# Kernel tuning notes

Measured on AMD Instinct MI355X. Metric: run time of the kernel, lower is better.

## Reference

```python
import jax, jax.numpy as jnp
from jax import lax
import numpy as np

IC, S, TS = 16, 3, 2  # inter_channels, num_subset_S, num_subset_T
EPS = 1e-5

def _ln2(x, g, b):
    # LayerNorm over last two dims (torch normalized_shape=[D1, D2])
    m = x.mean((-2, -1), keepdims=True)
    v = ((x - m) ** 2).mean((-2, -1), keepdims=True)
    return (x - m) / jnp.sqrt(v + EPS) * g + b

def _gelu(x):
    return jax.nn.gelu(x, approximate=False)

def setup_inputs() -> dict:
    key = jax.random.key(0)
    ks = jax.random.split(key, 12)
    N, V, T, C = 128, 25, 64, 64
    f = jnp.float32
    d = {}
    d['x'] = jax.random.normal(ks[0], (N, V, T, C), f)
    # spatial attention
    d['w_in_s'] = jax.random.normal(ks[1], (C, 2 * S * IC), f) * 0.05
    d['b_in_s'] = jnp.zeros((2 * S * IC,), f)
    d['alphas'] = jnp.ones((1, 1, 1, S), f)
    d['attention0s'] = jnp.ones((1, V, V, S), f) / V
    d['w_out_s'] = jax.random.normal(ks[2], (S * C, C), f) * 0.05
    d['b_out_s'] = jnp.zeros((C,), f)
    d['ln_out_s_g'] = jnp.ones((T, C), f)
    d['ln_out_s_b'] = jnp.zeros((T, C), f)
    d['w_ff_s'] = jax.random.normal(ks[3], (C, C), f) * 0.05
    d['b_ff_s'] = jnp.zeros((C,), f)
    d['ln_ff_s_g'] = jnp.ones((T, C), f)
    d['ln_ff_s_b'] = jnp.zeros((T, C), f)
    # temporal (directed) attention
    d['w_in_t'] = jax.random.normal(ks[4], (C, 4 * TS * IC), f) * 0.05
    d['b_in_t'] = jnp.zeros((4 * TS * IC,), f)
    d['alphat_f'] = jnp.ones((1, 1, 1, TS), f)
    d['alphat_b'] = jnp.ones((1, 1, 1, TS), f)
    d['w_out_t'] = jax.random.normal(ks[5], (2 * TS * C, C), f) * 0.05
    d['b_out_t'] = jnp.zeros((C,), f)
    d['ln_out_t_g'] = jnp.ones((V, C), f)
    d['ln_out_t_b'] = jnp.zeros((V, C), f)
    d['w_ff_t'] = jax.random.normal(ks[6], (C, C), f) * 0.05
    d['b_ff_t'] = jnp.zeros((C,), f)
    d['ln_ff_t_g'] = jnp.ones((V, C), f)
    d['ln_ff_t_b'] = jnp.zeros((V, C), f)
    # TCN tail: Conv2d(C, C, (7,1), pad (3,0)) + BatchNorm2d
    d['conv_w'] = jax.random.normal(ks[7], (C, C, 7, 1), f) * 0.05
    d['conv_b'] = jnp.zeros((C,), f)
    d['bn_g'] = jnp.ones((C,), f)
    d['bn_b'] = jnp.zeros((C,), f)
    return d

def reference(x, w_in_s, b_in_s, alphas, attention0s, w_out_s, b_out_s,
              ln_out_s_g, ln_out_s_b, w_ff_s, b_ff_s, ln_ff_s_g, ln_ff_s_b,
              w_in_t, b_in_t, alphat_f, alphat_b, w_out_t, b_out_t,
              ln_out_t_g, ln_out_t_b, w_ff_t, b_ff_t, ln_ff_t_g, ln_ff_t_b,
              conv_w, conv_b, bn_g, bn_b):
    N, V, T, C = x.shape
    # ---- spatial attention (tanh scores + global bias) ----
    qk = (x @ w_in_s + b_in_s).reshape(N, V, T, IC, 2 * S)
    q, k = qk[..., :S], qk[..., S:]
    att = jnp.tanh(jnp.einsum('nutcs,nvtcs->nuvs', q, k) / (IC * T)) * alphas + attention0s
    y = jnp.einsum('nutc,nuvs->nvtcs', x, att).reshape(N, V, T, S * C)
    y = _ln2(y @ w_out_s + b_out_s, ln_out_s_g, ln_out_s_b)
    y = _gelu(x + y)
    y = _gelu(x + _ln2(y @ w_ff_s + b_ff_s, ln_ff_s_g, ln_ff_s_b))
    y = y.transpose(0, 2, 1, 3)  # (N, T, V, C)
    # ---- directed temporal attention (causal masks) ----
    qkt = (y @ w_in_t + b_in_t).reshape(N, T, V, IC, 4 * TS)
    q_f, q_b = qkt[..., 0:TS], qkt[..., TS:2 * TS]
    k_f, k_b = qkt[..., 2 * TS:3 * TS], qkt[..., 3 * TS:]
    bmask = jnp.triu(jnp.ones((T, T), x.dtype))  # backward mask
    fmask = bmask.T                               # forward mask
    att_b = jnp.tanh(jnp.einsum('ntvcs,nqvcs->ntqs', q_b, k_b) / (IC * V)) * alphat_b
    att_f = jnp.tanh(jnp.einsum('ntvcs,nqvcs->ntqs', q_f, k_f) / (IC * V)) * alphat_f
    att_b = att_b * bmask[None, :, :, None]
    att_f = att_f * fmask[None, :, :, None]
    z_f = jnp.einsum('ntvc,ntqs->nqvcs', y, att_f).reshape(N, T, V, TS * C)
    z_b = jnp.einsum('ntvc,ntqs->nqvcs', y, att_b).reshape(N, T, V, TS * C)
    z = jnp.concatenate([z_f, z_b], axis=-1)  # (N, T, V, 2*TS*C)
    z = _ln2(z @ w_out_t + b_out_t, ln_out_t_g, ln_out_t_b)
    z = _gelu(y + z)
    z = _gelu(y + _ln2(z @ w_ff_t + b_ff_t, ln_ff_t_g, ln_ff_t_b))
    # ---- TCN tail: (N,T,V,C) -> (N,C,T,V) conv over T ----
    zc = z.transpose(0, 3, 1, 2)
    z1 = lax.conv_general_dilated(zc, conv_w, (1, 1), [(3, 3), (0, 0)],
                                  dimension_numbers=('NCHW', 'OIHW', 'NCHW'))
    z1 = z1 + conv_b[None, :, None, None]
    m = z1.mean((0, 2, 3), keepdims=True)
    v = ((z1 - m) ** 2).mean((0, 2, 3), keepdims=True)
    z1 = (z1 - m) / jnp.sqrt(v + EPS) * bn_g[None, :, None, None] + bn_b[None, :, None, None]
    z = _gelu(zc + z1)
    return z.transpose(0, 3, 2, 1)  # (N, C, T, V) -> (N, V, T, C)
```

## Files before the change

kernel.cpp:

```cpp
#include <hip/hip_runtime.h>
#include <math.h>

namespace {

constexpr int V_ = 25, T_ = 64, C_ = 64;

__device__ __forceinline__ float gelu_f(float x) {
  return 0.5f * x * (1.0f + erff(x * 0.7071067811865475f));
}

__device__ __forceinline__ float block_sum(float v, float* red, int tid) {
  red[tid] = v; __syncthreads();
#pragma unroll
  for (int o = 128; o > 0; o >>= 1) {
    if (tid < o) red[tid] += red[tid + o];
    __syncthreads();
  }
  float r = red[0]; __syncthreads();
  return r;
}

template <int NC>
__launch_bounds__(256, 2)
__global__ void gemm_k64(const float* __restrict__ A, const float* __restrict__ B,
                         const float* __restrict__ bias, float* __restrict__ C) {
  __shared__ float Al[64 * 68];
  __shared__ float Bl[64 * (NC + 4)];
  const int tid = threadIdx.x;
  const int row0 = blockIdx.x * 64;
  for (int i = tid; i < 4096; i += 256)
    Al[(i >> 6) * 68 + (i & 63)] = A[(size_t)(row0 + (i >> 6)) * 64 + (i & 63)];
  for (int i = tid; i < 64 * NC; i += 256) {
    int k = i / NC, c = i - k * NC;
    Bl[k * (NC + 4) + c] = B[i];
  }
  __syncthreads();
  const int ri = tid >> 5, cg = tid & 31;
  if (cg * 4 < NC) {
    float4 acc[8];
    float4 bf = *(const float4*)&bias[cg * 4];
#pragma unroll
    for (int i = 0; i < 8; ++i) acc[i] = bf;
    for (int k0 = 0; k0 < 64; k0 += 4) {
      float4 bv0 = *(const float4*)&Bl[(k0 + 0) * (NC + 4) + cg * 4];
      float4 bv1 = *(const float4*)&Bl[(k0 + 1) * (NC + 4) + cg * 4];
      float4 bv2 = *(const float4*)&Bl[(k0 + 2) * (NC + 4) + cg * 4];
      float4 bv3 = *(const float4*)&Bl[(k0 + 3) * (NC + 4) + cg * 4];
#pragma unroll
      for (int i = 0; i < 8; ++i) {
        float4 av = *(const float4*)&Al[(ri * 8 + i) * 68 + k0];
        acc[i].x += av.x * bv0.x + av.y * bv1.x + av.z * bv2.x + av.w * bv3.x;
        acc[i].y += av.x * bv0.y + av.y * bv1.y + av.z * bv2.y + av.w * bv3.y;
        acc[i].z += av.x * bv0.z + av.y * bv1.z + av.z * bv2.z + av.w * bv3.z;
        acc[i].w += av.x * bv0.w + av.y * bv1.w + av.z * bv2.w + av.w * bv3.w;
      }
    }
#pragma unroll
    for (int i = 0; i < 8; ++i)
      *(float4*)&C[(size_t)(row0 + ri * 8 + i) * NC + cg * 4] = acc[i];
  }
}

__global__ void att_s_kernel(const float* __restrict__ qk, const float* __restrict__ alphas,
                             const float* __restrict__ att0, float* __restrict__ att) {
  __shared__ float qs[4 * 3072];
  __shared__ float ks[3072];
  const int b = blockIdx.x, tid = threadIdx.x;
  const int n = b / 7, ug = b % 7;
  const int u0 = ug * 4;
  const int nu = (25 - u0 < 4) ? (25 - u0) : 4;
  for (int i = tid; i < nu * 3072; i += 256) {
    int ul = i / 3072, r = i - ul * 3072;
    int s = r >> 10, idx = r & 1023, t = idx >> 4, c = idx & 15;
    qs[i] = qk[(size_t)(n * 25 + u0 + ul) * 6144 + t * 96 + c * 6 + s];
  }
  const int ui = tid >> 6, l = tid & 63;
  const int u = u0 + ui;
  const float a0 = alphas[0], a1 = alphas[1], a2 = alphas[2];
  for (int v = 0; v < 25; ++v) {
    __syncthreads();
    for (int i = tid; i < 3072; i += 256) {
      int s = i >> 10, idx = i & 1023, t = idx >> 4, c = idx & 15;
      ks[i] = qk[(size_t)(n * 25 + v) * 6144 + t * 96 + c * 6 + 3 + s];
    }
    __syncthreads();
    if (u < 25) {
      float s0 = 0.f, s1 = 0.f, s2 = 0.f;
      for (int idx = l; idx < 1024; idx += 64) {
        s0 += qs[ui * 3072 + idx] * ks[idx];
        s1 += qs[ui * 3072 + 1024 + idx] * ks[1024 + idx];
        s2 += qs[ui * 3072 + 2048 + idx] * ks[2048 + idx];
      }
#pragma unroll
      for (int o = 32; o > 0; o >>= 1) {
        s0 += __shfl_down(s0, o);
        s1 += __shfl_down(s1, o);
        s2 += __shfl_down(s2, o);
      }
      if (l == 0) {
        float* dst = &att[(size_t)((n * 25 + u) * 25 + v) * 3];
        const float* ap = &att0[(u * 25 + v) * 3];
        dst[0] = tanhf(s0 * (1.f / 1024.f)) * a0 + ap[0];
        dst[1] = tanhf(s1 * (1.f / 1024.f)) * a1 + ap[1];
        dst[2] = tanhf(s2 * (1.f / 1024.f)) * a2 + ap[2];
      }
    }
  }
}

__launch_bounds__(256, 2)
__global__ void mix_gemm_s(const float* __restrict__ x, const float* __restrict__ att,
                           const float* __restrict__ w, const float* __restrict__ bias,
                           float* __restrict__ y2) {
  __shared__ float la[1875];
  __shared__ float xs[1600];
  __shared__ float y1l[25 * 194];
  __shared__ float wl[192 * 36];
  const int b = blockIdx.x, tid = threadIdx.x;
  const int n = b >> 6, t = b & 63;
  for (int i = tid; i < 1875; i += 256) la[i] = att[(size_t)n * 1875 + i];
  for (int i = tid; i < 1600; i += 256) {
    int u = i >> 6, c = i & 63;
    xs[i] = x[(size_t)((n * 25 + u) * 64 + t) * 64 + c];
  }
  __syncthreads();
  for (int slot = tid; slot < 400; slot += 256) {
    int v = slot >> 4, cg = slot & 15;
    float4 s0 = {0, 0, 0, 0}, s1 = {0, 0, 0, 0}, s2 = {0, 0, 0, 0};
    for (int u = 0; u < 25; ++u) {
      float4 xv = *(const float4*)&xs[u * 64 + cg * 4];
      const float* lp = &la[(u * 25 + v) * 3];
      float w0 = lp[0], w1 = lp[1], w2 = lp[2];
      s0.x += xv.x * w0; s0.y += xv.y * w0; s0.z += xv.z * w0; s0.w += xv.w * w0;
      s1.x += xv.x * w1; s1.y += xv.y * w1; s1.z += xv.z * w1; s1.w += xv.w * w1;
      s2.x += xv.x * w2; s2.y += xv.y * w2; s2.z += xv.z * w2; s2.w += xv.w * w2;
    }
    float* yp = &y1l[v * 194 + cg * 12];
    yp[0] = s0.x; yp[1] = s1.x; yp[2] = s2.x;
    yp[3] = s0.y; yp[4] = s1.y; yp[5] = s2.y;
    yp[6] = s0.z; yp[7] = s1.z; yp[8] = s2.z;
    yp[9] = s0.w; yp[10] = s1.w; yp[11] = s2.w;
  }
  for (int h = 0; h < 2; ++h) {
    __syncthreads();
    for (int i = tid; i < 192 * 32; i += 256) {
      int k = i >> 5, cc = i & 31;
      wl[k * 36 + cc] = w[k * 64 + h * 32 + cc];
    }
    __syncthreads();
    if (tid < 200) {
      int v = tid >> 3, cp = tid & 7;
      float4 acc = *(const float4*)&bias[h * 32 + cp * 4];
      for (int k = 0; k < 192; ++k) {
        float yv = y1l[v * 194 + k];
        float4 wv = *(const float4*)&wl[k * 36 + cp * 4];
        acc.x += yv * wv.x; acc.y += yv * wv.y; acc.z += yv * wv.z; acc.w += yv * wv.w;
      }
      *(float4*)&y2[(size_t)((n * 25 + v) * 64 + t) * 64 + h * 32 + cp * 4] = acc;
    }
  }
}

__global__ void lnln_s_kernel(const float* __restrict__ y2, const float* __restrict__ x,
                              const float* __restrict__ wff, const float* __restrict__ bff,
                              const float* __restrict__ g1, const float* __restrict__ b1,
                              const float* __restrict__ g2, const float* __restrict__ b2,
                              float* __restrict__ yt) {
  __shared__ float ya[64 * 66];
  __shared__ float wl[64 * 68];
  __shared__ float y6l[64 * 68];
  __shared__ float red[256];
  const int g = blockIdx.x, tid = threadIdx.x;
  const int n = g / 25, v = g % 25;
  const size_t base = (size_t)g * 4096;
  float s = 0.f;
  for (int i = tid; i < 4096; i += 256) {
    float val = y2[base + i];
    ya[(i >> 6) * 66 + (i & 63)] = val;
    s += val;
  }
  for (int i = tid; i < 4096; i += 256) wl[(i >> 6) * 68 + (i & 63)] = wff[i];
  float mean = block_sum(s, red, tid) * (1.f / 4096.f);
  float sq = 0.f;
  for (int i = tid; i < 4096; i += 256) {
    float d = ya[(i >> 6) * 66 + (i & 63)] - mean;
    sq += d * d;
  }
  float inv = rsqrtf(block_sum(sq, red, tid) * (1.f / 4096.f) + 1e-5f);
  for (int i = tid; i < 4096; i += 256) {
    int o = (i >> 6) * 66 + (i & 63);
    ya[o] = gelu_f(x[base + i] + (ya[o] - mean) * inv * g1[i] + b1[i]);
  }
  __syncthreads();
  const int ri = tid >> 4, ci = tid & 15;
  {
    float4 bf = *(const float4*)&bff[ci * 4];
    float4 acc[4];
#pragma unroll
    for (int i = 0; i < 4; ++i) acc[i] = bf;
    for (int k = 0; k < 64; ++k) {
      float4 wv = *(const float4*)&wl[k * 68 + ci * 4];
#pragma unroll
      for (int i = 0; i < 4; ++i) {
        float av = ya[(ri + 16 * i) * 66 + k];
        acc[i].x += av * wv.x; acc[i].y += av * wv.y;
        acc[i].z += av * wv.z; acc[i].w += av * wv.w;
      }
    }
#pragma unroll
    for (int i = 0; i < 4; ++i)
      *(float4*)&y6l[(ri + 16 * i) * 68 + ci * 4] = acc[i];
  }
  __syncthreads();
  float s2 = 0.f;
  for (int i = tid; i < 4096; i += 256) s2 += y6l[(i >> 6) * 68 + (i & 63)];
  float mean2 = block_sum(s2, red, tid) * (1.f / 4096.f);
  float sq2 = 0.f;
  for (int i = tid; i < 4096; i += 256) {
    float d = y6l[(i >> 6) * 68 + (i & 63)] - mean2;
    sq2 += d * d;
  }
  float inv2 = rsqrtf(block_sum(sq2, red, tid) * (1.f / 4096.f) + 1e-5f);
  for (int i = tid; i < 4096; i += 256) {
    int t = i >> 6, c = i & 63;
    yt[(size_t)((n * 64 + t) * 25 + v) * 64 + c] =
        gelu_f(x[base + i] + (y6l[t * 68 + c] - mean2) * inv2 * g2[i] + b2[i]);
  }
}

__global__ void att_t_kernel(const float* __restrict__ qkt, const float* __restrict__ af_al,
                             const float* __restrict__ ab_al, float* __restrict__ att4) {
  __shared__ float qs[8 * 1600];
  __shared__ float ks[1600];
  const int b = blockIdx.x, tid = threadIdx.x;
  const int n = b >> 3, to = b & 7;
  for (int i = tid; i < 8 * 1600; i += 256) {
    int tt = i / 1600, r = i - tt * 1600;
    int pair = r >> 2, j = r & 3, v = pair >> 4, c = pair & 15;
    qs[i] = qkt[(size_t)((n * 64 + to * 8 + tt) * 25 + v) * 128 + c * 8 + j];
  }
  const int tt = tid >> 5, l = tid & 31;
  const int t = to * 8 + tt;
  const float af0 = af_al[0], af1 = af_al[1], ab0 = ab_al[0], ab1 = ab_al[1];
  for (int q = 0; q < 64; ++q) {
    __syncthreads();
    for (int i = tid; i < 1600; i += 256) {
      int pair = i >> 2, j = i & 3, v = pair >> 4, c = pair & 15;
      ks[i] = qkt[(size_t)((n * 64 + q) * 25 + v) * 128 + c * 8 + 4 + j];
    }
    __syncthreads();
    float f0 = 0.f, f1 = 0.f, b0 = 0.f, b1 = 0.f;
    for (int idx = l; idx < 400; idx += 32) {
      float4 q4 = *(const float4*)&qs[tt * 1600 + idx * 4];
      float4 k4 = *(const float4*)&ks[idx * 4];
      f0 += q4.x * k4.x; f1 += q4.y * k4.y;
      b0 += q4.z * k4.z; b1 += q4.w * k4.w;
    }
#pragma unroll
    for (int o = 16; o > 0; o >>= 1) {
      f0 += __shfl_down(f0, o, 32); f1 += __shfl_down(f1, o, 32);
      b0 += __shfl_down(b0, o, 32); b1 += __shfl_down(b1, o, 32);
    }
    if (l == 0) {
      float mf = (q <= t) ? 1.f : 0.f;
      float mb = (q >= t) ? 1.f : 0.f;
      size_t o4 = ((size_t)(n * 4 + 0) * 64 + t) * 64 + q;
      att4[o4]           = tanhf(f0 * (1.f / 400.f)) * af0 * mf;
      att4[o4 + 4096]    = tanhf(f1 * (1.f / 400.f)) * af1 * mf;
      att4[o4 + 2 * 4096] = tanhf(b0 * (1.f / 400.f)) * ab0 * mb;
      att4[o4 + 3 * 4096] = tanhf(b1 * (1.f / 400.f)) * ab1 * mb;
    }
  }
}

__launch_bounds__(256, 2)
__global__ void mix_gemm_t(const float* __restrict__ yt, const float* __restrict__ att4,
                           const float* __restrict__ w, const float* __restrict__ bias,
                           float* __restrict__ z2) {
  __shared__ float smem[12288];
  float* as4 = smem;
  float* ys = smem + 8192;
  float* zvl = smem;
  const int b = blockIdx.x, tid = threadIdx.x;
  const int n = b / 50, r = b % 50;
  const int v = r >> 1, qh = r & 1;
  const int q0b = qh * 32;
  for (int i = tid; i < 8192; i += 256) {
    int sdi = i >> 11, t = (i >> 5) & 63, qq = i & 31;
    as4[i] = att4[((size_t)(n * 4 + sdi) * 64 + t) * 64 + q0b + qq];
  }
  for (int i = tid; i < 4096; i += 256) {
    int t = i >> 6, c = i & 63;
    ys[i] = yt[(size_t)((n * 64 + t) * 25 + v) * 64 + c];
  }
  __syncthreads();
  const int qg = tid >> 4, cg = tid & 15;
  const int q0 = qg * 2, c0 = cg * 4;
  float4 a00 = {0,0,0,0}, a01 = {0,0,0,0}, a10 = {0,0,0,0}, a11 = {0,0,0,0};
  float4 a20 = {0,0,0,0}, a21 = {0,0,0,0}, a30 = {0,0,0,0}, a31 = {0,0,0,0};
  for (int t = 0; t < 64; ++t) {
    float4 bv = *(const float4*)&ys[t * 64 + c0];
    float2 av0 = *(const float2*)&as4[(0 * 64 + t) * 32 + q0];
    float2 av1 = *(const float2*)&as4[(1 * 64 + t) * 32 + q0];
    float2 av2 = *(const float2*)&as4[(2 * 64 + t) * 32 + q0];
    float2 av3 = *(const float2*)&as4[(3 * 64 + t) * 32 + q0];
#define FMA4S(A, S) A.x += bv.x * (S); A.y += bv.y * (S); A.z += bv.z * (S); A.w += bv.w * (S)
    FMA4S(a00, av0.x); FMA4S(a01, av0.y);
    FMA4S(a10, av1.x); FMA4S(a11, av1.y);
    FMA4S(a20, av2.x); FMA4S(a21, av2.y);
    FMA4S(a30, av3.x); FMA4S(a31, av3.y);
#undef FMA4S
  }
  __syncthreads();
#define STORE_ZV(A, SDI, QI)                                                     \
  { int cb = ((SDI) >= 2 ? 128 : 0) + ((SDI) & 1);                               \
    float* zp = &zvl[(q0 + (QI)) * 258 + cb];                                    \
    zp[(c0 + 0) * 2] = A.x; zp[(c0 + 1) * 2] = A.y;                              \
    zp[(c0 + 2) * 2] = A.z; zp[(c0 + 3) * 2] = A.w; }
  STORE_ZV(a00, 0, 0); STORE_ZV(a01, 0, 1);
  STORE_ZV(a10, 1, 0); STORE_ZV(a11, 1, 1);
  STORE_ZV(a20, 2, 0); STORE_ZV(a21, 2, 1);
  STORE_ZV(a30, 3, 0); STORE_ZV(a31, 3, 1);
#undef STORE_ZV
  __syncthreads();
  const int qg2 = tid >> 6, cp = tid & 63;
  float acc2[8] = {0, 0, 0, 0, 0, 0, 0, 0};
  for (int col = 0; col < 256; ++col) {
    float wv = w[col * 64 + cp];
#pragma unroll
    for (int qi = 0; qi < 8; ++qi) acc2[qi] += zvl[(qg2 * 8 + qi) * 258 + col] * wv;
  }
  float bb = bias[cp];
#pragma unroll
  for (int qi = 0; qi < 8; ++qi)
    z2[(size_t)((n * 64 + q0b + qg2 * 8 + qi) * 25 + v) * 64 + cp] = acc2[qi] + bb;
}

__global__ void lnln_t_kernel(const float* __restrict__ z2, const float* __restrict__ ytr,
                              const float* __restrict__ wff, const float* __restrict__ bff,
                              const float* __restrict__ g1, const float* __restrict__ b1,
                              const float* __restrict__ g2, const float* __restrict__ b2,
                              float* __restrict__ zf) {
  __shared__ float za[25 * 66];
  __shared__ float yts[25 * 66];
  __shared__ float wl[64 * 68];
  __shared__ float z6l[25 * 68];
  __shared__ float red[256];
  const int g = blockIdx.x, tid = threadIdx.x;
  const size_t base = (size_t)g * 1600;
  float s = 0.f;
  for (int i = tid; i < 1600; i += 256) {
    float val = z2[base + i];
    za[(i >> 6) * 66 + (i & 63)] = val;
    yts[(i >> 6) * 66 + (i & 63)] = ytr[base + i];
    s += val;
  }
  for (int i = tid; i < 4096; i += 256) wl[(i >> 6) * 68 + (i & 63)] = wff[i];
  float mean = block_sum(s, red, tid) * (1.f / 1600.f);
  float sq = 0.f;
  for (int i = tid; i < 1600; i += 256) {
    float d = za[(i >> 6) * 66 + (i & 63)] - mean;
    sq += d * d;
  }
  float inv = rsqrtf(block_sum(sq, red, tid) * (1.f / 1600.f) + 1e-5f);
  for (int i = tid; i < 1600; i += 256) {
    int o = (i >> 6) * 66 + (i & 63);
    za[o] = gelu_f(yts[o] + (za[o] - mean) * inv * g1[i] + b1[i]);
  }
  __syncthreads();
  for (int slot = tid; slot < 400; slot += 256) {
    int v = slot >> 4, cq = slot & 15;
    float4 acc = *(const float4*)&bff[cq * 4];
    for (int k = 0; k < 64; ++k) {
      float av = za[v * 66 + k];
      float4 wv = *(const float4*)&wl[k * 68 + cq * 4];
      acc.x += av * wv.x; acc.y += av * wv.y; acc.z += av * wv.z; acc.w += av * wv.w;
    }
    *(float4*)&z6l[v * 68 + cq * 4] = acc;
  }
  __syncthreads();
  float s2 = 0.f;
  for (int i = tid; i < 1600; i += 256) s2 += z6l[(i >> 6) * 68 + (i & 63)];
  float mean2 = block_sum(s2, red, tid) * (1.f / 1600.f);
  float sq2 = 0.f;
  for (int i = tid; i < 1600; i += 256) {
    float d = z6l[(i >> 6) * 68 + (i & 63)] - mean2;
    sq2 += d * d;
  }
  float inv2 = rsqrtf(block_sum(sq2, red, tid) * (1.f / 1600.f) + 1e-5f);
  for (int i = tid; i < 1600; i += 256) {
    int o = (i >> 6) * 68 + (i & 63);
    zf[base + i] = gelu_f(yts[(i >> 6) * 66 + (i & 63)] + (z6l[o] - mean2) * inv2 * g2[i] + b2[i]);
  }
}

__global__ void convw_transpose(const float* __restrict__ w, float* __restrict__ wT) {
  int idx = blockIdx.x * 256 + threadIdx.x;
  if (idx < 64 * 64 * 7) {
    int dt = idx % 7, c = (idx / 7) % 64, cp = idx / 448;
    wT[(dt * 64 + c) * 64 + cp] = w[idx];
  }
}

__launch_bounds__(256, 2)
__global__ void conv_gemm(const float* __restrict__ zf, const float* __restrict__ wT,
                          const float* __restrict__ cb, float* __restrict__ z1,
                          float* __restrict__ part) {
  __shared__ float Al[128 * 68];
  __shared__ float Bl[64 * 68];
  const int tid = threadIdx.x;
  const int r0 = blockIdx.x * 128;
  const int ri = tid >> 4;
  const int cg = tid & 15;
  float4 acc[8];
  float4 bf = *(const float4*)&cb[cg * 4];
#pragma unroll
  for (int i = 0; i < 8; ++i) acc[i] = bf;
  for (int dt = 0; dt < 7; ++dt) {
    __syncthreads();
    for (int i = tid; i < 8192; i += 256) {
      int rl = i >> 6, c = i & 63;
      int grow = r0 + rl;
      int t = (grow % 1600) / 25;
      int tt = t + dt - 3;
      float val = 0.f;
      if (tt >= 0 && tt < 64)
        val = zf[(size_t)(grow + (dt - 3) * 25) * 64 + c];
      Al[rl * 68 + c] = val;
    }
    for (int i = tid; i < 4096; i += 256)
      Bl[(i >> 6) * 68 + (i & 63)] = wT[dt * 4096 + i];
    __syncthreads();
    for (int k0 = 0; k0 < 64; k0 += 4) {
      float4 bv0 = *(const float4*)&Bl[(k0 + 0) * 68 + cg * 4];
      float4 bv1 = *(const float4*)&Bl[(k0 + 1) * 68 + cg * 4];
      float4 bv2 = *(const float4*)&Bl[(k0 + 2) * 68 + cg * 4];
      float4 bv3 = *(const float4*)&Bl[(k0 + 3) * 68 + cg * 4];
#pragma unroll
      for (int i = 0; i < 8; ++i) {
        float4 av = *(const float4*)&Al[(ri + 16 * i) * 68 + k0];
        acc[i].x += av.x * bv0.x + av.y * bv1.x + av.z * bv2.x + av.w * bv3.x;
        acc[i].y += av.x * bv0.y + av.y * bv1.y + av.z * bv2.y + av.w * bv3.y;
        acc[i].z += av.x * bv0.z + av.y * bv1.z + av.z * bv2.z + av.w * bv3.z;
        acc[i].w += av.x * bv0.w + av.y * bv1.w + av.z * bv2.w + av.w * bv3.w;
      }
    }
  }
  float4 psum = {0, 0, 0, 0}, psq = {0, 0, 0, 0};
#pragma unroll
  for (int i = 0; i < 8; ++i) {
    *(float4*)&z1[(size_t)(r0 + ri + 16 * i) * 64 + cg * 4] = acc[i];
    psum.x += acc[i].x; psum.y += acc[i].y; psum.z += acc[i].z; psum.w += acc[i].w;
    psq.x += acc[i].x * acc[i].x; psq.y += acc[i].y * acc[i].y;
    psq.z += acc[i].z * acc[i].z; psq.w += acc[i].w * acc[i].w;
  }
  __syncthreads();
  *(float4*)&Al[ri * 68 + cg * 4] = psum;
  *(float4*)&Bl[ri * 68 + cg * 4] = psq;
  __syncthreads();
  if (tid < 64) {
    float s = 0.f, q = 0.f;
    for (int r = 0; r < 16; ++r) {
      s += Al[r * 68 + tid];
      q += Bl[r * 68 + tid];
    }
    part[(size_t)blockIdx.x * 128 + tid] = s;
    part[(size_t)blockIdx.x * 128 + 64 + tid] = q;
  }
}

__global__ void bn_final(const float* __restrict__ part, const float* __restrict__ g,
                         const float* __restrict__ bb, float* __restrict__ sc) {
  __shared__ float red[256], red2[256];
  const int c = blockIdx.x;
  const int tid = threadIdx.x;
  float s = 0.f, q = 0.f;
  for (int i = tid; i < 1600; i += 256) {
    s += part[(size_t)i * 128 + c];
    q += part[(size_t)i * 128 + 64 + c];
  }
  red[tid] = s;
  red2[tid] = q;
  __syncthreads();
#pragma unroll
  for (int o = 128; o > 0; o >>= 1) {
    if (tid < o) { red[tid] += red[tid + o]; red2[tid] += red2[tid + o]; }
    __syncthreads();
  }
  if (tid == 0) {
    const float M = 204800.f;
    float mean = red[0] / M;
    float var = red2[0] / M - mean * mean;
    float scale = g[c] * rsqrtf(var + 1e-5f);
    sc[c] = scale;
    sc[64 + c] = bb[c] - mean * scale;
  }
}

__global__ void final_kernel(const float* __restrict__ zf, const float* __restrict__ z1,
                             const float* __restrict__ sc, float* __restrict__ out) {
  const int b = blockIdx.x;
  const int n = b / 64, t = b % 64;
  const int tid = threadIdx.x;
  const size_t base = (size_t)(n * 64 + t) * 1600;
  for (int i = tid; i < 1600; i += 256) {
    int v = i >> 6, c = i & 63;
    float val = zf[base + i] + z1[base + i] * sc[c] + sc[64 + c];
    out[(size_t)((n * 25 + v) * 64 + t) * 64 + c] = gelu_f(val);
  }
}

}

extern "C" void kernel_launch(void* const* d_in, const int* in_sizes, int n_in,
                              void* d_out, int out_size, void* d_ws, size_t ws_size,
                              hipStream_t stream) {
  (void)in_sizes; (void)n_in; (void)out_size; (void)ws_size;
  const float* x          = (const float*)d_in[0];
  const float* w_in_s     = (const float*)d_in[1];
  const float* b_in_s     = (const float*)d_in[2];
  const float* alphas     = (const float*)d_in[3];
  const float* att0s      = (const float*)d_in[4];
  const float* w_out_s    = (const float*)d_in[5];
  const float* b_out_s    = (const float*)d_in[6];
  const float* ln_out_s_g = (const float*)d_in[7];
  const float* ln_out_s_b = (const float*)d_in[8];
  const float* w_ff_s     = (const float*)d_in[9];
  const float* b_ff_s     = (const float*)d_in[10];
  const float* ln_ff_s_g  = (const float*)d_in[11];
  const float* ln_ff_s_b  = (const float*)d_in[12];
  const float* w_in_t     = (const float*)d_in[13];
  const float* b_in_t     = (const float*)d_in[14];
  const float* alphat_f   = (const float*)d_in[15];
  const float* alphat_b   = (const float*)d_in[16];
  const float* w_out_t    = (const float*)d_in[17];
  const float* b_out_t    = (const float*)d_in[18];
  const float* ln_out_t_g = (const float*)d_in[19];
  const float* ln_out_t_b = (const float*)d_in[20];
  const float* w_ff_t     = (const float*)d_in[21];
  const float* b_ff_t     = (const float*)d_in[22];
  const float* ln_ff_t_g  = (const float*)d_in[23];
  const float* ln_ff_t_b  = (const float*)d_in[24];
  const float* conv_w     = (const float*)d_in[25];
  const float* conv_b     = (const float*)d_in[26];
  const float* bn_g       = (const float*)d_in[27];
  const float* bn_b       = (const float*)d_in[28];
  float* out = (float*)d_out;
  float* ws = (float*)d_ws;

  float* att4 = ws;
  float* part = ws;
  float* wT   = ws + 1048576;
  float* bnsc = ws + 1080000;
  float* qk   = ws + 2097152;
  float* y2   = ws + 2097152;
  float* qkt  = ws + 2097152;
  float* z1b  = ws + 2097152;
  float* yt   = ws + 28311552;
  float* zf   = ws + 41418752;
  float* att_s = out;
  float* z2    = out;

  dim3 blk(256);
  gemm_k64<96><<<3200, blk, 0, stream>>>(x, w_in_s, b_in_s, qk);
  att_s_kernel<<<128 * 7, blk, 0, stream>>>(qk, alphas, att0s, att_s);
  mix_gemm_s<<<8192, blk, 0, stream>>>(x, att_s, w_out_s, b_out_s, y2);
  lnln_s_kernel<<<3200, blk, 0, stream>>>(y2, x, w_ff_s, b_ff_s, ln_out_s_g, ln_out_s_b,
                                          ln_ff_s_g, ln_ff_s_b, yt);
  gemm_k64<128><<<3200, blk, 0, stream>>>(yt, w_in_t, b_in_t, qkt);
  att_t_kernel<<<128 * 8, blk, 0, stream>>>(qkt, alphat_f, alphat_b, att4);
  mix_gemm_t<<<6400, blk, 0, stream>>>(yt, att4, w_out_t, b_out_t, z2);
  lnln_t_kernel<<<8192, blk, 0, stream>>>(z2, yt, w_ff_t, b_ff_t, ln_out_t_g, ln_out_t_b,
                                          ln_ff_t_g, ln_ff_t_b, zf);
  convw_transpose<<<112, blk, 0, stream>>>(conv_w, wT);
  conv_gemm<<<1600, blk, 0, stream>>>(zf, wT, conv_b, z1b, part);
  bn_final<<<64, blk, 0, stream>>>(part, bn_g, bn_b, bnsc);
  final_kernel<<<8192, blk, 0, stream>>>(zf, z1b, bnsc, out);
}
```

Baseline: 2.596 ms.

## Split attention-mix and output projection into separate mix and tiled GEMM kernels

```diff
diff --git a/kernel.cpp b/kernel.cpp
--- a/kernel.cpp
+++ b/kernel.cpp
@@ -2,8 +2,6 @@
 #include <math.h>
 
 namespace {
-
-constexpr int V_ = 25, T_ = 64, C_ = 64;
 
 __device__ __forceinline__ float gelu_f(float x) {
   return 0.5f * x * (1.0f + erff(x * 0.7071067811865475f));
@@ -61,6 +59,76 @@
   }
 }
 
+template <int KT>
+__launch_bounds__(256, 3)
+__global__ void gemm_kn(const float* __restrict__ A, const float* __restrict__ Bp,
+                        const float* __restrict__ bias, float* __restrict__ C) {
+  __shared__ float Al[128 * 68];
+  __shared__ float Bl[64 * 68];
+  const int tid = threadIdx.x;
+  const int r0 = blockIdx.x * 128;
+  const int rowg = tid >> 3, colg = tid & 7, c0 = colg * 8;
+  float4 acc[4][2];
+  {
+    float4 b0 = *(const float4*)&bias[c0];
+    float4 b1 = *(const float4*)&bias[c0 + 4];
+#pragma unroll
+    for (int i = 0; i < 4; ++i) { acc[i][0] = b0; acc[i][1] = b1; }
+  }
+  for (int kc = 0; kc < KT / 64; ++kc) {
+    __syncthreads();
+    for (int i = tid; i < 8192; i += 256) {
+      int rl = i >> 6, k = i & 63;
+      Al[rl * 68 + k] = A[(size_t)(r0 + rl) * KT + kc * 64 + k];
+    }
+    for (int i = tid; i < 4096; i += 256)
+      Bl[(i >> 6) * 68 + (i & 63)] = Bp[(size_t)kc * 4096 + i];
+    __syncthreads();
+    for (int k0 = 0; k0 < 64; k0 += 4) {
+      float4 bb[4][2];
+#pragma unroll
+      for (int k = 0; k < 4; ++k) {
+        bb[k][0] = *(const float4*)&Bl[(k0 + k) * 68 + c0];
+        bb[k][1] = *(const float4*)&Bl[(k0 + k) * 68 + c0 + 4];
+      }
+#pragma unroll
+      for (int i = 0; i < 4; ++i) {
+        float4 av = *(const float4*)&Al[(rowg + 32 * i) * 68 + k0];
+#pragma unroll
+        for (int h = 0; h < 2; ++h) {
+          acc[i][h].x += av.x * bb[0][h].x + av.y * bb[1][h].x + av.z * bb[2][h].x + av.w * bb[3][h].x;
+          acc[i][h].y += av.x * bb[0][h].y + av.y * bb[1][h].y + av.z * bb[2][h].y + av.w * bb[3][h].y;
+          acc[i][h].z += av.x * bb[0][h].z + av.y * bb[1][h].z + av.z * bb[2][h].z + av.w * bb[3][h].z;
+          acc[i][h].w += av.x * bb[0][h].w + av.y * bb[1][h].w + av.z * bb[2][h].w + av.w * bb[3][h].w;
+        }
+      }
+    }
+  }
+#pragma unroll
+  for (int i = 0; i < 4; ++i) {
+    *(float4*)&C[(size_t)(r0 + rowg + 32 * i) * 64 + c0] = acc[i][0];
+    *(float4*)&C[(size_t)(r0 + rowg + 32 * i) * 64 + c0 + 4] = acc[i][1];
+  }
+}
+
+__global__ void permute_ws_k(const float* __restrict__ w, float* __restrict__ wp) {
+  int i = blockIdx.x * 256 + threadIdx.x;
+  if (i < 12288) {
+    int row = i >> 6, cc = i & 63;
+    int s = row >> 6, c = row & 63;
+    wp[i] = w[(c * 3 + s) * 64 + cc];
+  }
+}
+
+__global__ void permute_wt_k(const float* __restrict__ w, float* __restrict__ wp) {
+  int i = blockIdx.x * 256 + threadIdx.x;
+  if (i < 16384) {
+    int row = i >> 6, cc = i & 63;
+    int dir = row >> 7, r2 = row & 127, s = r2 >> 6, c = r2 & 63;
+    wp[i] = w[(dir * 128 + c * 2 + s) * 64 + cc];
+  }
+}
+
 __global__ void att_s_kernel(const float* __restrict__ qk, const float* __restrict__ alphas,
                              const float* __restrict__ att0, float* __restrict__ att) {
   __shared__ float qs[4 * 3072];
@@ -108,55 +176,58 @@
   }
 }
 
-__launch_bounds__(256, 2)
-__global__ void mix_gemm_s(const float* __restrict__ x, const float* __restrict__ att,
-                           const float* __restrict__ w, const float* __restrict__ bias,
-                           float* __restrict__ y2) {
-  __shared__ float la[1875];
-  __shared__ float xs[1600];
-  __shared__ float y1l[25 * 194];
-  __shared__ float wl[192 * 36];
+__launch_bounds__(256, 3)
+__global__ void mix_s_y1(const float* __restrict__ x, const float* __restrict__ att,
+                         float* __restrict__ y1) {
+  __shared__ float ap[625 * 4];
+  __shared__ float xs[4 * 25 * 68];
   const int b = blockIdx.x, tid = threadIdx.x;
-  const int n = b >> 6, t = b & 63;
-  for (int i = tid; i < 1875; i += 256) la[i] = att[(size_t)n * 1875 + i];
-  for (int i = tid; i < 1600; i += 256) {
-    int u = i >> 6, c = i & 63;
-    xs[i] = x[(size_t)((n * 25 + u) * 64 + t) * 64 + c];
-  }
-  __syncthreads();
-  for (int slot = tid; slot < 400; slot += 256) {
-    int v = slot >> 4, cg = slot & 15;
-    float4 s0 = {0, 0, 0, 0}, s1 = {0, 0, 0, 0}, s2 = {0, 0, 0, 0};
+  const int n = b >> 4, tq = b & 15;
+  for (int i = tid; i < 1875; i += 256) {
+    int u = i / 75, rem = i - u * 75, v = rem / 3, s = rem - v * 3;
+    ap[(v * 25 + u) * 4 + s] = att[(size_t)n * 1875 + i];
+  }
+  for (int i = tid; i < 6400; i += 256) {
+    int tl = i / 1600, r = i - tl * 1600, u = r >> 6, c = r & 63;
+    xs[(tl * 25 + u) * 68 + c] = x[(size_t)((n * 25 + u) * 64 + tq * 4 + tl) * 64 + c];
+  }
+  __syncthreads();
+  if (tid < 200) {
+    const int v = tid >> 3, c0 = (tid & 7) * 8;
+    float4 acc[4][3][2];
+#pragma unroll
+    for (int tl = 0; tl < 4; ++tl)
+#pragma unroll
+      for (int s = 0; s < 3; ++s) {
+        acc[tl][s][0] = make_float4(0.f, 0.f, 0.f, 0.f);
+        acc[tl][s][1] = make_float4(0.f, 0.f, 0.f, 0.f);
+      }
     for (int u = 0; u < 25; ++u) {
-      float4 xv = *(const float4*)&xs[u * 64 + cg * 4];
-      const float* lp = &la[(u * 25 + v) * 3];
-      float w0 = lp[0], w1 = lp[1], w2 = lp[2];
-      s0.x += xv.x * w0; s0.y += xv.y * w0; s0.z += xv.z * w0; s0.w += xv.w * w0;
-      s1.x += xv.x * w1; s1.y += xv.y * w1; s1.z += xv.z * w1; s1.w += xv.w * w1;
-      s2.x += xv.x * w2; s2.y += xv.y * w2; s2.z += xv.z * w2; s2.w += xv.w * w2;
-    }
-    float* yp = &y1l[v * 194 + cg * 12];
-    yp[0] = s0.x; yp[1] = s1.x; yp[2] = s2.x;
-    yp[3] = s0.y; yp[4] = s1.y; yp[5] = s2.y;
-    yp[6] = s0.z; yp[7] = s1.z; yp[8] = s2.z;
-    yp[9] = s0.w; yp[10] = s1.w; yp[11] = s2.w;
-  }
-  for (int h = 0; h < 2; ++h) {
-    __syncthreads();
-    for (int i = tid; i < 192 * 32; i += 256) {
-      int k = i >> 5, cc = i & 31;
-      wl[k * 36 + cc] = w[k * 64 + h * 32 + cc];
-    }
-    __syncthreads();
-    if (tid < 200) {
-      int v = tid >> 3, cp = tid & 7;
-      float4 acc = *(const float4*)&bias[h * 32 + cp * 4];
-      for (int k = 0; k < 192; ++k) {
-        float yv = y1l[v * 194 + k];
-        float4 wv = *(const float4*)&wl[k * 36 + cp * 4];
-        acc.x += yv * wv.x; acc.y += yv * wv.y; acc.z += yv * wv.z; acc.w += yv * wv.w;
-      }
-      *(float4*)&y2[(size_t)((n * 25 + v) * 64 + t) * 64 + h * 32 + cp * 4] = acc;
+      float4 a = *(const float4*)&ap[(v * 25 + u) * 4];
+#pragma unroll
+      for (int tl = 0; tl < 4; ++tl) {
+        const float* xp = &xs[(tl * 25 + u) * 68 + c0];
+        float4 x0 = *(const float4*)&xp[0];
+        float4 x1 = *(const float4*)&xp[4];
+#define MIXFMA(S, AS)                                                        \
+  acc[tl][S][0].x += x0.x * AS; acc[tl][S][0].y += x0.y * AS;                \
+  acc[tl][S][0].z += x0.z * AS; acc[tl][S][0].w += x0.w * AS;                \
+  acc[tl][S][1].x += x1.x * AS; acc[tl][S][1].y += x1.y * AS;                \
+  acc[tl][S][1].z += x1.z * AS; acc[tl][S][1].w += x1.w * AS
+        MIXFMA(0, a.x);
+        MIXFMA(1, a.y);
+        MIXFMA(2, a.z);
+#undef MIXFMA
+      }
+    }
+#pragma unroll
+    for (int tl = 0; tl < 4; ++tl) {
+      float* yp = &y1[(size_t)((n * 25 + v) * 64 + tq * 4 + tl) * 192];
+#pragma unroll
+      for (int s = 0; s < 3; ++s) {
+        *(float4*)&yp[s * 64 + c0] = acc[tl][s][0];
+        *(float4*)&yp[s * 64 + c0 + 4] = acc[tl][s][1];
+      }
     }
   }
 }
@@ -265,8 +336,8 @@
       float mf = (q <= t) ? 1.f : 0.f;
       float mb = (q >= t) ? 1.f : 0.f;
       size_t o4 = ((size_t)(n * 4 + 0) * 64 + t) * 64 + q;
-      att4[o4]           = tanhf(f0 * (1.f / 400.f)) * af0 * mf;
-      att4[o4 + 4096]    = tanhf(f1 * (1.f / 400.f)) * af1 * mf;
+      att4[o4]            = tanhf(f0 * (1.f / 400.f)) * af0 * mf;
+      att4[o4 + 4096]     = tanhf(f1 * (1.f / 400.f)) * af1 * mf;
       att4[o4 + 2 * 4096] = tanhf(b0 * (1.f / 400.f)) * ab0 * mb;
       att4[o4 + 3 * 4096] = tanhf(b1 * (1.f / 400.f)) * ab1 * mb;
     }
@@ -274,15 +345,14 @@
 }
 
 __launch_bounds__(256, 2)
-__global__ void mix_gemm_t(const float* __restrict__ yt, const float* __restrict__ att4,
-                           const float* __restrict__ w, const float* __restrict__ bias,
-                           float* __restrict__ z2) {
+__global__ void mix_t_zv(const float* __restrict__ yt, const float* __restrict__ att4,
+                         float* __restrict__ zv, int n0) {
   __shared__ float smem[12288];
   float* as4 = smem;
   float* ys = smem + 8192;
-  float* zvl = smem;
   const int b = blockIdx.x, tid = threadIdx.x;
-  const int n = b / 50, r = b % 50;
+  const int nl = b / 50, r = b % 50;
+  const int n = n0 + nl;
   const int v = r >> 1, qh = r & 1;
   const int q0b = qh * 32;
   for (int i = tid; i < 8192; i += 256) {
@@ -311,29 +381,14 @@
     FMA4S(a30, av3.x); FMA4S(a31, av3.y);
 #undef FMA4S
   }
-  __syncthreads();
-#define STORE_ZV(A, SDI, QI)                                                     \
-  { int cb = ((SDI) >= 2 ? 128 : 0) + ((SDI) & 1);                               \
-    float* zp = &zvl[(q0 + (QI)) * 258 + cb];                                    \
-    zp[(c0 + 0) * 2] = A.x; zp[(c0 + 1) * 2] = A.y;                              \
-    zp[(c0 + 2) * 2] = A.z; zp[(c0 + 3) * 2] = A.w; }
+#define STORE_ZV(A, SDI, QI)                                                  \
+  *(float4*)&zv[(size_t)((nl * 64 + q0b + q0 + (QI)) * 25 + v) * 256 +        \
+                ((SDI) >> 1) * 128 + ((SDI) & 1) * 64 + c0] = A
   STORE_ZV(a00, 0, 0); STORE_ZV(a01, 0, 1);
   STORE_ZV(a10, 1, 0); STORE_ZV(a11, 1, 1);
   STORE_ZV(a20, 2, 0); STORE_ZV(a21, 2, 1);
   STORE_ZV(a30, 3, 0); STORE_ZV(a31, 3, 1);
 #undef STORE_ZV
-  __syncthreads();
-  const int qg2 = tid >> 6, cp = tid & 63;
-  float acc2[8] = {0, 0, 0, 0, 0, 0, 0, 0};
-  for (int col = 0; col < 256; ++col) {
-    float wv = w[col * 64 + cp];
-#pragma unroll
-    for (int qi = 0; qi < 8; ++qi) acc2[qi] += zvl[(qg2 * 8 + qi) * 258 + col] * wv;
-  }
-  float bb = bias[cp];
-#pragma unroll
-  for (int qi = 0; qi < 8; ++qi)
-    z2[(size_t)((n * 64 + q0b + qg2 * 8 + qi) * 25 + v) * 64 + cp] = acc2[qi] + bb;
 }
 
 __global__ void lnln_t_kernel(const float* __restrict__ z2, const float* __restrict__ ytr,
@@ -550,29 +605,39 @@
 
   float* att4 = ws;
   float* part = ws;
-  float* wT   = ws + 1048576;
-  float* bnsc = ws + 1080000;
   float* qk   = ws + 2097152;
-  float* y2   = ws + 2097152;
+  float* y1   = ws + 2097152;
   float* qkt  = ws + 2097152;
+  float* zv   = ws + 2097152;
   float* z1b  = ws + 2097152;
   float* yt   = ws + 28311552;
   float* zf   = ws + 41418752;
+  float* wT   = ws + 54525952;
+  float* bnsc = ws + 54554624;
+  float* wp_s = ws + 54554752;
+  float* wp_t = ws + 54567040;
   float* att_s = out;
+  float* y2    = out;
   float* z2    = out;
 
   dim3 blk(256);
+  permute_ws_k<<<48, blk, 0, stream>>>(w_out_s, wp_s);
+  permute_wt_k<<<64, blk, 0, stream>>>(w_out_t, wp_t);
+  convw_transpose<<<112, blk, 0, stream>>>(conv_w, wT);
   gemm_k64<96><<<3200, blk, 0, stream>>>(x, w_in_s, b_in_s, qk);
   att_s_kernel<<<128 * 7, blk, 0, stream>>>(qk, alphas, att0s, att_s);
-  mix_gemm_s<<<8192, blk, 0, stream>>>(x, att_s, w_out_s, b_out_s, y2);
+  mix_s_y1<<<2048, blk, 0, stream>>>(x, att_s, y1);
+  gemm_kn<192><<<1600, blk, 0, stream>>>(y1, wp_s, b_out_s, y2);
   lnln_s_kernel<<<3200, blk, 0, stream>>>(y2, x, w_ff_s, b_ff_s, ln_out_s_g, ln_out_s_b,
                                           ln_ff_s_g, ln_ff_s_b, yt);
   gemm_k64<128><<<3200, blk, 0, stream>>>(yt, w_in_t, b_in_t, qkt);
   att_t_kernel<<<128 * 8, blk, 0, stream>>>(qkt, alphat_f, alphat_b, att4);
-  mix_gemm_t<<<6400, blk, 0, stream>>>(yt, att4, w_out_t, b_out_t, z2);
+  for (int h = 0; h < 2; ++h) {
+    mix_t_zv<<<3200, blk, 0, stream>>>(yt, att4, zv, h * 64);
+    gemm_kn<256><<<800, blk, 0, stream>>>(zv, wp_t, b_out_t, z2 + (size_t)h * 6553600);
+  }
   lnln_t_kernel<<<8192, blk, 0, stream>>>(z2, yt, w_ff_t, b_ff_t, ln_out_t_g, ln_out_t_b,
                                           ln_ff_t_g, ln_ff_t_b, zf);
-  convw_transpose<<<112, blk, 0, stream>>>(conv_w, wT);
   conv_gemm<<<1600, blk, 0, stream>>>(zf, wT, conv_b, z1b, part);
   bn_final<<<64, blk, 0, stream>>>(part, bn_g, bn_b, bnsc);
   final_kernel<<<8192, blk, 0, stream>>>(zf, z1b, bnsc, out);
```

Result: faster. 2.152 ms (-17.1%).
